# Performance work log

Hardware: AMD Instinct MI355X
Metric: run time of the kernel (lower is better)

Reference implementation:

```python
import jax, jax.numpy as jnp
import numpy as np

B, A = 262144, 128          # observations, max assortment size
N = B * A                   # total item universe (disjoint assortments)
LN10 = float(np.log(10.0))  # original uses torch.log10


def setup_inputs() -> dict:
    key = jax.random.key(0)
    k1, k2 = jax.random.split(key)
    x = jax.random.normal(k1, (N,), dtype=jnp.float32)          # item utilities
    idx = jnp.arange(N, dtype=jnp.int32).reshape(B, A)          # padded ragged assortment indices
    lengths = jax.random.randint(k2, (B,), 1, A + 1, dtype=jnp.int32)  # valid lengths per row
    # exactly one chosen item per assortment: position 0 (always within length >= 1)
    y = jnp.zeros((N,), jnp.float32).at[idx[:, 0]].set(1.0)
    return {"x": x, "y": y, "idx": idx, "lengths": lengths}


def reference(x, y, idx, lengths):
    A_ = idx.shape[1]
    # ragged validity mask [B, A]
    mask = jnp.arange(A_) < jnp.clip(lengths, 1, A_)[:, None]
    xs = x[idx]                                  # [B, A] gathered utilities
    ys = y[idx]                                  # [B, A] gathered choice indicators
    # log10(exp(x_chosen) / sum_j exp(x_j)) == (x_chosen - logsumexp) / ln(10)
    logits = jnp.where(mask, xs, -jnp.inf)
    lse = jax.nn.logsumexp(logits, axis=1)       # [B]
    x_chosen = jnp.sum(jnp.where(mask & (ys == 1.0), xs, 0.0), axis=1)  # [B]
    log10_prob = (x_chosen - lse) / LN10
    return -jnp.mean(log10_prob)
```

## Files before the change

### kernel.cpp

```cpp
#include <hip/hip_runtime.h>
#include <math.h>

#define B_ROWS 262144
#define A_COLS 128
#define LN10F  2.302585092994046f

#define NBLK            2048
#define ROWS_PER_BLOCK  (B_ROWS / NBLK)
#define ROWS_PER_WAVE   (ROWS_PER_BLOCK / 4)
#define RGROUP          4
#define NITER           (ROWS_PER_WAVE / RGROUP)

__global__ __launch_bounds__(256) void mnl_row_kernel(
    const float* __restrict__ x,
    const float* __restrict__ y,
    const int*   __restrict__ idx,
    const int*   __restrict__ lengths,
    float*       __restrict__ partials)
{
    const int wave  = threadIdx.x >> 6;
    const int lane  = threadIdx.x & 63;
    const int wrow0 = blockIdx.x * ROWS_PER_BLOCK + wave * ROWS_PER_WAVE;

    float acc_cs  = 0.0f;
    float acc_log = 0.0f;

    for (int it = 0; it < NITER; ++it) {
        const int r0 = wrow0 + it * RGROUP;
        const int4 L4 = *(const int4*)(lengths + r0);
        const int len[RGROUP] = { L4.x, L4.y, L4.z, L4.w };

        int i0[RGROUP], i1[RGROUP];
        #pragma unroll
        for (int r = 0; r < RGROUP; ++r) {
            const long base = (long)(r0 + r) * A_COLS;
            i0[r] = idx[base + lane];
            i1[r] = idx[base + 64 + lane];
        }

        float xv0[RGROUP], xv1[RGROUP], yv0[RGROUP], yv1[RGROUP];
        #pragma unroll
        for (int r = 0; r < RGROUP; ++r) {
            xv0[r] = x[i0[r]];  yv0[r] = y[i0[r]];
            xv1[r] = x[i1[r]];  yv1[r] = y[i1[r]];
        }

        #pragma unroll
        for (int r = 0; r < RGROUP; ++r) {
            const int  l  = min(max(len[r], 1), A_COLS);
            const bool m0 = lane < l;
            const bool m1 = (lane + 64) < l;

            float s = 0.0f;
            if (m0) { s += __expf(xv0[r]); if (yv0[r] == 1.0f) acc_cs += xv0[r]; }
            if (m1) { s += __expf(xv1[r]); if (yv1[r] == 1.0f) acc_cs += xv1[r]; }

            #pragma unroll
            for (int off = 32; off > 0; off >>= 1)
                s += __shfl_xor(s, off, 64);

            if (lane == 0) acc_log += __logf(s);
        }
    }

    #pragma unroll
    for (int off = 32; off > 0; off >>= 1)
        acc_cs += __shfl_xor(acc_cs, off, 64);

    __shared__ float part[4];
    if (lane == 0) part[wave] = acc_cs - acc_log;
    __syncthreads();
    if (threadIdx.x == 0)
        partials[blockIdx.x] = part[0] + part[1] + part[2] + part[3];
}

__global__ __launch_bounds__(256) void mnl_reduce_kernel(
    const float* __restrict__ partials,
    float*       __restrict__ out)
{
    __shared__ float sdata[256];
    float s = 0.0f;
    for (int i = threadIdx.x; i < NBLK; i += 256)
        s += partials[i];
    sdata[threadIdx.x] = s;
    __syncthreads();
    for (int st = 128; st > 0; st >>= 1) {
        if (threadIdx.x < st) sdata[threadIdx.x] += sdata[threadIdx.x + st];
        __syncthreads();
    }
    if (threadIdx.x == 0)
        out[0] = -sdata[0] / ((float)B_ROWS * LN10F);
}

extern "C" void kernel_launch(void* const* d_in, const int* in_sizes, int n_in,
                              void* d_out, int out_size, void* d_ws, size_t ws_size,
                              hipStream_t stream) {
    const float* x       = (const float*)d_in[0];
    const float* y       = (const float*)d_in[1];
    const int*   idx     = (const int*)d_in[2];
    const int*   lengths = (const int*)d_in[3];
    float* out      = (float*)d_out;
    float* partials = (float*)d_ws;

    mnl_row_kernel<<<NBLK, 256, 0, stream>>>(x, y, idx, lengths, partials);
    mnl_reduce_kernel<<<1, 256, 0, stream>>>(partials, out);
}
```

Baseline: 356.5 us.

## Vectorize idx loads, split waves into half-wave rows, and issue all gathers up front

Each half-wave now handles one row, with lanes loading four indices as an int4 and gathering four x/y values. All loads for eight rows per wave are issued before any compute, and the grid grows to 8192 blocks so more memory requests are in flight. The chosen-item test becomes an fma with y, which assumes y is a 0/1 indicator. The per-row log is computed redundantly across 32 lanes and rescaled when combining.

After: 353.1 us. No clear change (-1.0%).

```diff
diff --git a/kernel.cpp b/kernel.cpp
--- a/kernel.cpp
+++ b/kernel.cpp
@@ -5,70 +5,71 @@
 #define A_COLS 128
 #define LN10F  2.302585092994046f
 
-#define NBLK            2048
-#define ROWS_PER_BLOCK  (B_ROWS / NBLK)
-#define ROWS_PER_WAVE   (ROWS_PER_BLOCK / 4)
-#define RGROUP          4
-#define NITER           (ROWS_PER_WAVE / RGROUP)
+#define NBLK           8192
+#define ROWS_PER_BLOCK 32
+#define PAIRS          4
 
 __global__ __launch_bounds__(256) void mnl_row_kernel(
     const float* __restrict__ x,
     const float* __restrict__ y,
-    const int*   __restrict__ idx,
+    const int4*  __restrict__ idx4,
     const int*   __restrict__ lengths,
     float*       __restrict__ partials)
 {
-    const int wave  = threadIdx.x >> 6;
-    const int lane  = threadIdx.x & 63;
-    const int wrow0 = blockIdx.x * ROWS_PER_BLOCK + wave * ROWS_PER_WAVE;
+    const int wave = threadIdx.x >> 6;
+    const int lane = threadIdx.x & 63;
+    const int half = lane >> 5;
+    const int l32  = lane & 31;
+    const int r0   = blockIdx.x * ROWS_PER_BLOCK + wave * (2 * PAIRS);
 
-    float acc_cs  = 0.0f;
+    int  len[PAIRS];
+    int4 iv[PAIRS];
+    #pragma unroll
+    for (int p = 0; p < PAIRS; ++p) {
+        const int row = r0 + 2 * p + half;
+        len[p] = lengths[row];
+        iv[p]  = idx4[row * (A_COLS / 4) + l32];
+    }
+
+    float xs[PAIRS][4], ys[PAIRS][4];
+    #pragma unroll
+    for (int p = 0; p < PAIRS; ++p) {
+        xs[p][0] = x[iv[p].x]; xs[p][1] = x[iv[p].y];
+        xs[p][2] = x[iv[p].z]; xs[p][3] = x[iv[p].w];
+        ys[p][0] = y[iv[p].x]; ys[p][1] = y[iv[p].y];
+        ys[p][2] = y[iv[p].z]; ys[p][3] = y[iv[p].w];
+    }
+
+    const int c0 = l32 * 4;
+    float acc_cs = 0.0f;
     float acc_log = 0.0f;
 
-    for (int it = 0; it < NITER; ++it) {
-        const int r0 = wrow0 + it * RGROUP;
-        const int4 L4 = *(const int4*)(lengths + r0);
-        const int len[RGROUP] = { L4.x, L4.y, L4.z, L4.w };
-
-        int i0[RGROUP], i1[RGROUP];
+    #pragma unroll
+    for (int p = 0; p < PAIRS; ++p) {
+        const int L = min(max(len[p], 1), A_COLS);
+        float s = 0.0f;
         #pragma unroll
-        for (int r = 0; r < RGROUP; ++r) {
-            const long base = (long)(r0 + r) * A_COLS;
-            i0[r] = idx[base + lane];
-            i1[r] = idx[base + 64 + lane];
+        for (int k = 0; k < 4; ++k) {
+            if (c0 + k < L) {
+                s += __expf(xs[p][k]);
+                acc_cs = fmaf(ys[p][k], xs[p][k], acc_cs);
+            }
         }
-
-        float xv0[RGROUP], xv1[RGROUP], yv0[RGROUP], yv1[RGROUP];
-        #pragma unroll
-        for (int r = 0; r < RGROUP; ++r) {
-            xv0[r] = x[i0[r]];  yv0[r] = y[i0[r]];
-            xv1[r] = x[i1[r]];  yv1[r] = y[i1[r]];
-        }
-
-        #pragma unroll
-        for (int r = 0; r < RGROUP; ++r) {
-            const int  l  = min(max(len[r], 1), A_COLS);
-            const bool m0 = lane < l;
-            const bool m1 = (lane + 64) < l;
-
-            float s = 0.0f;
-            if (m0) { s += __expf(xv0[r]); if (yv0[r] == 1.0f) acc_cs += xv0[r]; }
-            if (m1) { s += __expf(xv1[r]); if (yv1[r] == 1.0f) acc_cs += xv1[r]; }
-
-            #pragma unroll
-            for (int off = 32; off > 0; off >>= 1)
-                s += __shfl_xor(s, off, 64);
-
-            if (lane == 0) acc_log += __logf(s);
-        }
+        s += __shfl_xor(s, 16, 64);
+        s += __shfl_xor(s,  8, 64);
+        s += __shfl_xor(s,  4, 64);
+        s += __shfl_xor(s,  2, 64);
+        s += __shfl_xor(s,  1, 64);
+        acc_log += __logf(s);
     }
 
+    float v = acc_cs - acc_log * 0.03125f;
     #pragma unroll
     for (int off = 32; off > 0; off >>= 1)
-        acc_cs += __shfl_xor(acc_cs, off, 64);
+        v += __shfl_xor(v, off, 64);
 
     __shared__ float part[4];
-    if (lane == 0) part[wave] = acc_cs - acc_log;
+    if (lane == 0) part[wave] = v;
     __syncthreads();
     if (threadIdx.x == 0)
         partials[blockIdx.x] = part[0] + part[1] + part[2] + part[3];
@@ -97,11 +98,11 @@
                               hipStream_t stream) {
     const float* x       = (const float*)d_in[0];
     const float* y       = (const float*)d_in[1];
-    const int*   idx     = (const int*)d_in[2];
+    const int4*  idx4    = (const int4*)d_in[2];
     const int*   lengths = (const int*)d_in[3];
     float* out      = (float*)d_out;
     float* partials = (float*)d_ws;
 
-    mnl_row_kernel<<<NBLK, 256, 0, stream>>>(x, y, idx, lengths, partials);
+    mnl_row_kernel<<<NBLK, 256, 0, stream>>>(x, y, idx4, lengths, partials);
     mnl_reduce_kernel<<<1, 256, 0, stream>>>(partials, out);
 }
```
